# Kernel tuning notes

Measured on AMD Instinct MI355X. Metric: run time of the kernel, lower is better.

## Reference

```python
import jax, jax.numpy as jnp
import numpy as np

U, I, NG, D, G, B = 100000, 50000, 20000, 64, 20, 16384
H_GE = (D + 2 * D) // 2  # 96, group_encoder hidden

def setup_inputs() -> dict:
    key = jax.random.key(0)
    ks = jax.random.split(key, 24)
    s = 0.1
    return {
        'group_inputs': jax.random.randint(ks[0], (B,), 0, NG),
        'item_inputs': jax.random.randint(ks[1], (B,), 0, I),
        'group_members': jax.random.randint(ks[2], (NG, G), 0, U),
        'eps': jax.random.normal(ks[3], (B, D), dtype=jnp.float32),
        'user_emb': jax.random.normal(ks[4], (U, D), dtype=jnp.float32) * s,
        'item_emb': jax.random.normal(ks[5], (I, D), dtype=jnp.float32) * s,
        # user_encoder: MLP(D, D, 1) -> Linear(D,D), ReLU, Linear(D,D)
        'ue_w1': jax.random.normal(ks[6], (D, D), dtype=jnp.float32) * s,
        'ue_b1': jnp.zeros((D,), jnp.float32),
        'ue_w2': jax.random.normal(ks[7], (D, D), dtype=jnp.float32) * s,
        'ue_b2': jnp.zeros((D,), jnp.float32),
        # group_encoder: MLP(D, 2D, 1) -> Linear(D,96), ReLU, Linear(96,2D)
        'ge_w1': jax.random.normal(ks[8], (D, H_GE), dtype=jnp.float32) * s,
        'ge_b1': jnp.zeros((H_GE,), jnp.float32),
        'ge_w2': jax.random.normal(ks[9], (H_GE, 2 * D), dtype=jnp.float32) * s,
        'ge_b2': jnp.zeros((2 * D,), jnp.float32),
        # attention: Linear(2D,16), ReLU, Linear(16,1)
        'at_w1': jax.random.normal(ks[10], (2 * D, 16), dtype=jnp.float32) * s,
        'at_b1': jnp.zeros((16,), jnp.float32),
        'at_w2': jax.random.normal(ks[11], (16, 1), dtype=jnp.float32) * s,
        'at_b2': jnp.zeros((1,), jnp.float32),
        # predict: Linear(3D,8), ReLU, Linear(8,1)
        'pr_w1': jax.random.normal(ks[12], (3 * D, 8), dtype=jnp.float32) * s,
        'pr_b1': jnp.zeros((8,), jnp.float32),
        'pr_w2': jax.random.normal(ks[13], (8, 1), dtype=jnp.float32) * s,
        'pr_b2': jnp.zeros((1,), jnp.float32),
    }

def reference(group_inputs, item_inputs, group_members, eps,
              user_emb, item_emb,
              ue_w1, ue_b1, ue_w2, ue_b2,
              ge_w1, ge_b1, ge_w2, ge_b2,
              at_w1, at_b1, at_w2, at_b2,
              pr_w1, pr_b1, pr_w2, pr_b2):
    mem_idx = group_members[group_inputs]              # [B, G]
    me = user_emb[mem_idx]                             # [B, G, D] gather
    # user encoder MLP
    enc = jnp.maximum(me @ ue_w1 + ue_b1, 0) @ ue_w2 + ue_b2
    gz = jnp.maximum(jnp.mean(enc, axis=1), 0)         # [B, D]
    gz = jnp.maximum(gz @ ge_w1 + ge_b1, 0) @ ge_w2 + ge_b2  # [B, 2D]
    z_mu, log_sigma = gz[:, :D], gz[:, D:]
    z_sigma = 0.1 + 0.9 * jax.nn.sigmoid(log_sigma)
    ie = item_emb[item_inputs]                          # [B, D]
    gi = jnp.concatenate([me, jnp.broadcast_to(ie[:, None, :], me.shape)], axis=-1)  # [B, G, 2D]
    score = jnp.maximum(gi @ at_w1 + at_b1, 0) @ at_w2 + at_b2  # [B, G, 1]
    w = jax.nn.softmax(score[..., 0], axis=1)           # [B, G]
    g_att = jnp.einsum('bg,bgd->bd', w, me)             # [B, D]
    ge_full = g_att + z_mu + z_sigma * eps              # sample_z with given eps
    ncf = jnp.concatenate([ge_full * ie, ge_full, ie], axis=-1)  # [B, 3D]
    h = jnp.maximum(ncf @ pr_w1 + pr_b1, 0) @ pr_w2 + pr_b2
    return jax.nn.sigmoid(h)                            # [B, 1]
```

## Files before the change

kernel.cpp:

```cpp
#include <hip/hip_runtime.h>
#include <math.h>

#define D_   64
#define G_   20
#define BT   16
#define XPAD 132

typedef __attribute__((ext_vector_type(8))) short bf8;
typedef __attribute__((ext_vector_type(4))) float f4;

__device__ __forceinline__ short f2bf(float f){
    union { float f; unsigned u; } c; c.f = f;
    unsigned r = c.u + 0x7fffu + ((c.u >> 16) & 1u);
    return (short)(r >> 16);
}
__device__ __forceinline__ bf8 pack8(float4 a, float4 b){
    bf8 r;
    r[0]=f2bf(a.x); r[1]=f2bf(a.y); r[2]=f2bf(a.z); r[3]=f2bf(a.w);
    r[4]=f2bf(b.x); r[5]=f2bf(b.y); r[6]=f2bf(b.z); r[7]=f2bf(b.w);
    return r;
}

__global__ __launch_bounds__(256, 4) void vargr_mfma_kernel(
    const int*   __restrict__ group_inputs,
    const int*   __restrict__ item_inputs,
    const int*   __restrict__ group_members,
    const float* __restrict__ eps,
    const float* __restrict__ user_emb,
    const float* __restrict__ item_emb,
    const float* __restrict__ ue_w1, const float* __restrict__ ue_b1,
    const float* __restrict__ ue_w2, const float* __restrict__ ue_b2,
    const float* __restrict__ ge_w1, const float* __restrict__ ge_b1,
    const float* __restrict__ ge_w2, const float* __restrict__ ge_b2,
    const float* __restrict__ at_w1, const float* __restrict__ at_b1,
    const float* __restrict__ at_w2, const float* __restrict__ at_b2,
    const float* __restrict__ pr_w1, const float* __restrict__ pr_b1,
    const float* __restrict__ pr_w2, const float* __restrict__ pr_b2,
    float* __restrict__ out)
{
    __shared__ unsigned short Wt[80*64];
    __shared__ float xA[BT*XPAD];
    __shared__ float xB[BT*XPAD];
    __shared__ float ieb[BT*64];
    __shared__ float gefb[BT*64];
    __shared__ float tvs[BT*16];
    __shared__ float wsm[BT*G_];
    __shared__ int   sidx[BT*G_];

    const int tid = threadIdx.x;
    const int w = tid >> 6, l = tid & 63;
    const int bbase = blockIdx.x * BT;

    for (int e = tid; e < 64*80; e += 256){
        int k = e / 80, col = e - k*80;
        float v = (col < 64) ? ue_w1[k*64 + col] : at_w1[k*16 + (col - 64)];
        int byte = col*128 + ( ((2*k) & ~15) ^ ((col & 7) << 4) ) + ((2*k) & 15);
        *(unsigned short*)((char*)Wt + byte) = (unsigned short)f2bf(v);
    }

    {
        int bb = 4*w + (l >> 4);
        int q  = l & 15;
        int item = item_inputs[bbase + bb];
        ((float4*)(ieb + bb*64))[q] = ((const float4*)(item_emb + (size_t)item*64))[q];
    }
    #pragma unroll
    for (int i = 0; i < 4; ++i){
        int bb = 4*w + i;
        if (l < G_){
            int gid = group_inputs[bbase + bb];
            sidx[bb*G_ + l] = group_members[gid*G_ + l];
        }
    }
    {
        int bb = 4*w + (l >> 4);
        int u  = l & 15;
        float acc = at_b1[u];
        const float* ier = ieb + bb*64;
        #pragma unroll 8
        for (int k = 0; k < 64; ++k) acc += ier[k] * at_w1[(64 + k)*16 + u];
        tvs[bb*16 + u] = acc;
    }
    __syncthreads();

    bf8 bfr[5][2];
    #pragma unroll
    for (int nt = 0; nt < 5; ++nt)
        #pragma unroll
        for (int kt = 0; kt < 2; ++kt){
            int col  = nt*16 + (l & 15);
            int byte = col*128 + ( (kt*64 + (l >> 4)*16) ^ ((col & 7) << 4) );
            bfr[nt][kt] = *(const bf8*)((const char*)Wt + byte);
        }
    float bias1[4];
    #pragma unroll
    for (int nt = 0; nt < 4; ++nt) bias1[nt] = ue_b1[nt*16 + (l & 15)];
    const float aw2  = at_w2[l & 15];
    const float atb2 = at_b2[0];

    #pragma unroll 1
    for (int i = 0; i < 4; ++i){
        const int bb = 4*w + i;
        const int* sx = sidx + bb*G_;
        float msum[4] = {0.f, 0.f, 0.f, 0.f};

        #pragma unroll
        for (int mt = 0; mt < 2; ++mt){
            int r = mt*16 + (l & 15);
            int g = (r < G_) ? r : (G_ - 1);
            const float4* p = (const float4*)(user_emb + (size_t)sx[g]*64) + ((l >> 4)*2);
            bf8 a0 = pack8(p[0], p[1]);
            bf8 a1 = pack8(p[8], p[9]);

            f4 acc[5];
            #pragma unroll
            for (int nt = 0; nt < 5; ++nt) acc[nt] = (f4){0.f, 0.f, 0.f, 0.f};
            #pragma unroll
            for (int nt = 0; nt < 5; ++nt){
                acc[nt] = __builtin_amdgcn_mfma_f32_16x16x32_bf16(a0, bfr[nt][0], acc[nt], 0, 0, 0);
                acc[nt] = __builtin_amdgcn_mfma_f32_16x16x32_bf16(a1, bfr[nt][1], acc[nt], 0, 0, 0);
            }

            #pragma unroll
            for (int nt = 0; nt < 4; ++nt){
                float rs = 0.f;
                #pragma unroll
                for (int rr = 0; rr < 4; ++rr) rs += fmaxf(acc[nt][rr] + bias1[nt], 0.f);
                if (mt == 1 && (l >> 4) != 0) rs = 0.f;
                msum[nt] += rs;
            }
            {
                float tvv = tvs[bb*16 + (l & 15)];
                float vv[4];
                #pragma unroll
                for (int rr = 0; rr < 4; ++rr) vv[rr] = fmaxf(acc[4][rr] + tvv, 0.f) * aw2;
                #pragma unroll
                for (int rr = 0; rr < 4; ++rr){
                    vv[rr] += __shfl_xor(vv[rr], 1);
                    vv[rr] += __shfl_xor(vv[rr], 2);
                    vv[rr] += __shfl_xor(vv[rr], 4);
                    vv[rr] += __shfl_xor(vv[rr], 8);
                }
                if ((l & 15) == 0 && (mt == 0 || (l >> 4) == 0)){
                    #pragma unroll
                    for (int rr = 0; rr < 4; ++rr)
                        wsm[bb*G_ + mt*16 + (l >> 4)*4 + rr] = vv[rr] + atb2;
                }
            }
        }

        #pragma unroll
        for (int nt = 0; nt < 4; ++nt){
            msum[nt] += __shfl_xor(msum[nt], 16);
            msum[nt] += __shfl_xor(msum[nt], 32);
            if ((l >> 4) == nt) xA[bb*XPAD + nt*16 + (l & 15)] = msum[nt] * (1.f / G_);
        }

        {
            float sval = (l < G_) ? wsm[bb*G_ + l] : -3.0e38f;
            float mx = sval;
            mx = fmaxf(mx, __shfl_xor(mx, 1, 32));
            mx = fmaxf(mx, __shfl_xor(mx, 2, 32));
            mx = fmaxf(mx, __shfl_xor(mx, 4, 32));
            mx = fmaxf(mx, __shfl_xor(mx, 8, 32));
            mx = fmaxf(mx, __shfl_xor(mx, 16, 32));
            float e = (l < G_) ? expf(sval - mx) : 0.f;
            float sm = e;
            sm += __shfl_xor(sm, 1, 32);
            sm += __shfl_xor(sm, 2, 32);
            sm += __shfl_xor(sm, 4, 32);
            sm += __shfl_xor(sm, 8, 32);
            sm += __shfl_xor(sm, 16, 32);
            if (l < G_) wsm[bb*G_ + l] = e / sm;
        }

        {
            float ga = 0.f;
            #pragma unroll
            for (int g = 0; g < G_; ++g)
                ga += wsm[bb*G_ + g] * user_emb[(size_t)sx[g]*64 + l];
            gefb[bb*64 + l] = ga;
        }
    }
    __syncthreads();

    {
        int col = w*16 + (l & 15);
        f4 acc = (f4){0.f, 0.f, 0.f, 0.f};
        #pragma unroll
        for (int kt = 0; kt < 2; ++kt){
            const float* ap = xA + (l & 15)*XPAD + kt*32 + (l >> 4)*8;
            bf8 a = pack8(*(const float4*)ap, *(const float4*)(ap + 4));
            int k0 = kt*32 + (l >> 4)*8;
            bf8 bfrg;
            #pragma unroll
            for (int q = 0; q < 8; ++q) bfrg[q] = f2bf(ue_w2[(k0 + q)*64 + col]);
            acc = __builtin_amdgcn_mfma_f32_16x16x32_bf16(a, bfrg, acc, 0, 0, 0);
        }
        float bs = ue_b2[col];
        #pragma unroll
        for (int rr = 0; rr < 4; ++rr)
            xB[(4*(l >> 4) + rr)*XPAD + col] = fmaxf(acc[rr] + bs, 0.f);
    }
    __syncthreads();

    for (int t = w; t < 6; t += 4){
        int col = t*16 + (l & 15);
        f4 acc = (f4){0.f, 0.f, 0.f, 0.f};
        #pragma unroll
        for (int kt = 0; kt < 2; ++kt){
            const float* ap = xB + (l & 15)*XPAD + kt*32 + (l >> 4)*8;
            bf8 a = pack8(*(const float4*)ap, *(const float4*)(ap + 4));
            int k0 = kt*32 + (l >> 4)*8;
            bf8 bfrg;
            #pragma unroll
            for (int q = 0; q < 8; ++q) bfrg[q] = f2bf(ge_w1[(k0 + q)*96 + col]);
            acc = __builtin_amdgcn_mfma_f32_16x16x32_bf16(a, bfrg, acc, 0, 0, 0);
        }
        float bs = ge_b1[col];
        #pragma unroll
        for (int rr = 0; rr < 4; ++rr)
            xA[(4*(l >> 4) + rr)*XPAD + col] = fmaxf(acc[rr] + bs, 0.f);
    }
    __syncthreads();

    for (int t = w; t < 8; t += 4){
        int col = t*16 + (l & 15);
        f4 acc = (f4){0.f, 0.f, 0.f, 0.f};
        #pragma unroll
        for (int kt = 0; kt < 3; ++kt){
            const float* ap = xA + (l & 15)*XPAD + kt*32 + (l >> 4)*8;
            bf8 a = pack8(*(const float4*)ap, *(const float4*)(ap + 4));
            int k0 = kt*32 + (l >> 4)*8;
            bf8 bfrg;
            #pragma unroll
            for (int q = 0; q < 8; ++q) bfrg[q] = f2bf(ge_w2[(k0 + q)*128 + col]);
            acc = __builtin_amdgcn_mfma_f32_16x16x32_bf16(a, bfrg, acc, 0, 0, 0);
        }
        float bs = ge_b2[col];
        #pragma unroll
        for (int rr = 0; rr < 4; ++rr)
            xB[(4*(l >> 4) + rr)*XPAD + col] = acc[rr] + bs;
    }
    __syncthreads();

    {
        float pa[8], pb_[8], pc_[8], pb1v[8], pw2v[8];
        #pragma unroll
        for (int u = 0; u < 8; ++u){
            pa[u]   = pr_w1[l*8 + u];
            pb_[u]  = pr_w1[(64 + l)*8 + u];
            pc_[u]  = pr_w1[(128 + l)*8 + u];
            pb1v[u] = pr_b1[u];
            pw2v[u] = pr_w2[u];
        }
        const float pb2v = pr_b2[0];

        #pragma unroll 1
        for (int i = 0; i < 4; ++i){
            int bb = 4*w + i;
            int b  = bbase + bb;
            float muv = xB[bb*XPAD + l];
            float sgr = xB[bb*XPAD + 64 + l];
            float sg  = 0.1f + 0.9f / (1.f + expf(-sgr));
            float gefv = gefb[bb*64 + l] + muv + sg * eps[(size_t)b*64 + l];
            float iev  = ieb[bb*64 + l];
            float x0 = gefv * iev;
            float pu[8];
            #pragma unroll
            for (int u = 0; u < 8; ++u) pu[u] = x0*pa[u] + gefv*pb_[u] + iev*pc_[u];
            #pragma unroll
            for (int off = 1; off < 64; off <<= 1){
                #pragma unroll
                for (int u = 0; u < 8; ++u) pu[u] += __shfl_xor(pu[u], off);
            }
            float hh = 0.f;
            #pragma unroll
            for (int u = 0; u < 8; ++u) hh += fmaxf(pu[u] + pb1v[u], 0.f) * pw2v[u];
            if (l == 0) out[b] = 1.f / (1.f + expf(-(hh + pb2v)));
        }
    }
}

extern "C" void kernel_launch(void* const* d_in, const int* in_sizes, int n_in,
                              void* d_out, int out_size, void* d_ws, size_t ws_size,
                              hipStream_t stream) {
    const int*   group_inputs  = (const int*)d_in[0];
    const int*   item_inputs   = (const int*)d_in[1];
    const int*   group_members = (const int*)d_in[2];
    const float* eps           = (const float*)d_in[3];
    const float* user_emb      = (const float*)d_in[4];
    const float* item_emb      = (const float*)d_in[5];
    const float* ue_w1 = (const float*)d_in[6];
    const float* ue_b1 = (const float*)d_in[7];
    const float* ue_w2 = (const float*)d_in[8];
    const float* ue_b2 = (const float*)d_in[9];
    const float* ge_w1 = (const float*)d_in[10];
    const float* ge_b1 = (const float*)d_in[11];
    const float* ge_w2 = (const float*)d_in[12];
    const float* ge_b2 = (const float*)d_in[13];
    const float* at_w1 = (const float*)d_in[14];
    const float* at_b1 = (const float*)d_in[15];
    const float* at_w2 = (const float*)d_in[16];
    const float* at_b2 = (const float*)d_in[17];
    const float* pr_w1 = (const float*)d_in[18];
    const float* pr_b1 = (const float*)d_in[19];
    const float* pr_w2 = (const float*)d_in[20];
    const float* pr_b2 = (const float*)d_in[21];
    float* out = (float*)d_out;

    const int nb = in_sizes[0];
    vargr_mfma_kernel<<<nb / BT, 256, 0, stream>>>(
        group_inputs, item_inputs, group_members, eps, user_emb, item_emb,
        ue_w1, ue_b1, ue_w2, ue_b2, ge_w1, ge_b1, ge_w2, ge_b2,
        at_w1, at_b1, at_w2, at_b2, pr_w1, pr_b1, pr_w2, pr_b2,
        out);
}
```

Baseline: 45.06 us.

## Pre-pack weights to bf16 MFMA fragments in a prep kernel and restructure member tiling

Adds a small prep kernel that converts all MLP weights once into bf16 MFMA fragment layout in workspace, so each block loads fragments directly instead of building a swizzled LDS copy and converting weights per block. Member tiling now computes members 0-15 per batch row in the loop and handles members 16-19 of four rows together in one extra MFMA tile, removing the half-empty second tile. Item attention projection, intermediate activations (stored as bf16) and the final predict MLP now use MFMA instead of scalar loops and 64-lane shuffle reductions. It costs an extra kernel launch and more bf16 rounding in intermediate layers.

```diff
diff --git a/kernel.cpp b/kernel.cpp
--- a/kernel.cpp
+++ b/kernel.cpp
@@ -1,161 +1,234 @@
 #include <hip/hip_runtime.h>
+#include <hip/hip_bf16.h>
 #include <math.h>
 
-#define D_   64
 #define G_   20
 #define BT   16
-#define XPAD 132
 
 typedef __attribute__((ext_vector_type(8))) short bf8;
 typedef __attribute__((ext_vector_type(4))) float f4;
 
-__device__ __forceinline__ short f2bf(float f){
-    union { float f; unsigned u; } c; c.f = f;
-    unsigned r = c.u + 0x7fffu + ((c.u >> 16) & 1u);
-    return (short)(r >> 16);
+#define FMB  0
+#define FAT  10
+#define FUE2 12
+#define FGE1 20
+#define FGE2 32
+#define FPR  56
+#define FTOT 62
+
+__device__ __forceinline__ unsigned cvt2(float x, float y){
+    float2 f; f.x = x; f.y = y;
+    __hip_bfloat162 h = __float22bfloat162_rn(f);
+    return *reinterpret_cast<unsigned*>(&h);
+}
+__device__ __forceinline__ unsigned short cvt1(float x){
+    __hip_bfloat16 h = __float2bfloat16(x);
+    return *reinterpret_cast<unsigned short*>(&h);
 }
 __device__ __forceinline__ bf8 pack8(float4 a, float4 b){
-    bf8 r;
-    r[0]=f2bf(a.x); r[1]=f2bf(a.y); r[2]=f2bf(a.z); r[3]=f2bf(a.w);
-    r[4]=f2bf(b.x); r[5]=f2bf(b.y); r[6]=f2bf(b.z); r[7]=f2bf(b.w);
-    return r;
-}
-
-__global__ __launch_bounds__(256, 4) void vargr_mfma_kernel(
+    union { bf8 v; unsigned u[4]; } t;
+    t.u[0] = cvt2(a.x, a.y); t.u[1] = cvt2(a.z, a.w);
+    t.u[2] = cvt2(b.x, b.y); t.u[3] = cvt2(b.z, b.w);
+    return t.v;
+}
+
+__global__ __launch_bounds__(256) void vargr_prep(
+    const float* __restrict__ ue_w1, const float* __restrict__ ue_w2,
+    const float* __restrict__ ge_w1, const float* __restrict__ ge_w2,
+    const float* __restrict__ at_w1, const float* __restrict__ pr_w1,
+    unsigned short* __restrict__ ws)
+{
+    int f = blockIdx.x * 256 + threadIdx.x;
+    if (f >= FTOT * 64) return;
+    int lane = f & 63, grp = f >> 6;
+    int col = lane & 15;
+    int q8  = (lane >> 4) * 8;
+    float v[8];
+    if (grp < FAT){
+        int g = grp - FMB; int nt = g >> 1; int k0 = (g & 1)*32 + q8; int c = nt*16 + col;
+        #pragma unroll
+        for (int q = 0; q < 8; ++q)
+            v[q] = (c < 64) ? ue_w1[(k0+q)*64 + c] : at_w1[(k0+q)*16 + (c - 64)];
+    } else if (grp < FUE2){
+        int g = grp - FAT; int k0 = g*32 + q8;
+        #pragma unroll
+        for (int q = 0; q < 8; ++q) v[q] = at_w1[(64 + k0 + q)*16 + col];
+    } else if (grp < FGE1){
+        int g = grp - FUE2; int nt = g >> 1; int k0 = (g & 1)*32 + q8;
+        #pragma unroll
+        for (int q = 0; q < 8; ++q) v[q] = ue_w2[(k0+q)*64 + nt*16 + col];
+    } else if (grp < FGE2){
+        int g = grp - FGE1; int nt = g >> 1; int k0 = (g & 1)*32 + q8;
+        #pragma unroll
+        for (int q = 0; q < 8; ++q) v[q] = ge_w1[(k0+q)*96 + nt*16 + col];
+    } else if (grp < FPR){
+        int g = grp - FGE2; int nt = g / 3; int k0 = (g % 3)*32 + q8;
+        #pragma unroll
+        for (int q = 0; q < 8; ++q) v[q] = ge_w2[(k0+q)*128 + nt*16 + col];
+    } else {
+        int g = grp - FPR; int k0 = g*32 + q8;
+        #pragma unroll
+        for (int q = 0; q < 8; ++q) v[q] = (col < 8) ? pr_w1[(k0+q)*8 + col] : 0.f;
+    }
+    union { bf8 b; unsigned u[4]; } t;
+    t.u[0] = cvt2(v[0], v[1]); t.u[1] = cvt2(v[2], v[3]);
+    t.u[2] = cvt2(v[4], v[5]); t.u[3] = cvt2(v[6], v[7]);
+    *reinterpret_cast<bf8*>(ws + (size_t)f * 8) = t.b;
+}
+
+__global__ __launch_bounds__(256, 4) void vargr_main(
     const int*   __restrict__ group_inputs,
     const int*   __restrict__ item_inputs,
     const int*   __restrict__ group_members,
     const float* __restrict__ eps,
     const float* __restrict__ user_emb,
     const float* __restrict__ item_emb,
-    const float* __restrict__ ue_w1, const float* __restrict__ ue_b1,
-    const float* __restrict__ ue_w2, const float* __restrict__ ue_b2,
-    const float* __restrict__ ge_w1, const float* __restrict__ ge_b1,
-    const float* __restrict__ ge_w2, const float* __restrict__ ge_b2,
-    const float* __restrict__ at_w1, const float* __restrict__ at_b1,
-    const float* __restrict__ at_w2, const float* __restrict__ at_b2,
-    const float* __restrict__ pr_w1, const float* __restrict__ pr_b1,
+    const float* __restrict__ ue_b1, const float* __restrict__ ue_b2,
+    const float* __restrict__ ge_b1, const float* __restrict__ ge_b2,
+    const float* __restrict__ at_b1, const float* __restrict__ at_w2,
+    const float* __restrict__ at_b2, const float* __restrict__ pr_b1,
     const float* __restrict__ pr_w2, const float* __restrict__ pr_b2,
+    const unsigned short* __restrict__ ws,
     float* __restrict__ out)
 {
-    __shared__ unsigned short Wt[80*64];
-    __shared__ float xA[BT*XPAD];
-    __shared__ float xB[BT*XPAD];
-    __shared__ float ieb[BT*64];
+    __shared__ unsigned short xAh[BT*136];
+    __shared__ unsigned short xBh[BT*136];
+    __shared__ float ieb[BT*68];
     __shared__ float gefb[BT*64];
-    __shared__ float tvs[BT*16];
     __shared__ float wsm[BT*G_];
     __shared__ int   sidx[BT*G_];
+    __shared__ float x3u[BT*132];
 
     const int tid = threadIdx.x;
     const int w = tid >> 6, l = tid & 63;
+    const int lq = l >> 4, lr = l & 15;
     const int bbase = blockIdx.x * BT;
-
-    for (int e = tid; e < 64*80; e += 256){
-        int k = e / 80, col = e - k*80;
-        float v = (col < 64) ? ue_w1[k*64 + col] : at_w1[k*16 + (col - 64)];
-        int byte = col*128 + ( ((2*k) & ~15) ^ ((col & 7) << 4) ) + ((2*k) & 15);
-        *(unsigned short*)((char*)Wt + byte) = (unsigned short)f2bf(v);
-    }
+    const bf8* wsf = (const bf8*)ws;
+
+    bf8 bfr[5][2];
+    #pragma unroll
+    for (int nt = 0; nt < 5; ++nt)
+        #pragma unroll
+        for (int kt = 0; kt < 2; ++kt)
+            bfr[nt][kt] = wsf[(FMB + nt*2 + kt)*64 + l];
+    bf8 abot0 = wsf[(FAT + 0)*64 + l];
+    bf8 abot1 = wsf[(FAT + 1)*64 + l];
+
+    float bias1[4];
+    #pragma unroll
+    for (int nt = 0; nt < 4; ++nt) bias1[nt] = ue_b1[nt*16 + lr];
+    const float aw2  = at_w2[lr];
+    const float atb2 = at_b2[0];
 
     {
-        int bb = 4*w + (l >> 4);
-        int q  = l & 15;
+        int bb = 4*w + lq;
         int item = item_inputs[bbase + bb];
-        ((float4*)(ieb + bb*64))[q] = ((const float4*)(item_emb + (size_t)item*64))[q];
-    }
-    #pragma unroll
-    for (int i = 0; i < 4; ++i){
-        int bb = 4*w + i;
-        if (l < G_){
+        ((float4*)(ieb + bb*68))[lr] = ((const float4*)(item_emb + (size_t)item*64))[lr];
+    }
+    if (l < G_){
+        #pragma unroll
+        for (int i = 0; i < 4; ++i){
+            int bb = 4*w + i;
             int gid = group_inputs[bbase + bb];
             sidx[bb*G_ + l] = group_members[gid*G_ + l];
         }
     }
+    __syncthreads();
+
+    f4 tvacc = (f4){0.f, 0.f, 0.f, 0.f};
+    #pragma unroll
+    for (int kt = 0; kt < 2; ++kt){
+        const float* ap = ieb + lr*68 + kt*32 + lq*8;
+        bf8 a = pack8(*(const float4*)ap, *(const float4*)(ap + 4));
+        tvacc = __builtin_amdgcn_mfma_f32_16x16x32_bf16(a, kt ? abot1 : abot0, tvacc, 0, 0, 0);
+    }
+    const float atb1 = at_b1[lr];
+    float tvi[4];
+    #pragma unroll
+    for (int i = 0; i < 4; ++i)
+        tvi[i] = __shfl(tvacc[i], w*16 + lr) + atb1;
+
+    float rem[4];
     {
-        int bb = 4*w + (l >> 4);
-        int u  = l & 15;
-        float acc = at_b1[u];
-        const float* ier = ieb + bb*64;
-        #pragma unroll 8
-        for (int k = 0; k < 64; ++k) acc += ier[k] * at_w1[(64 + k)*16 + u];
-        tvs[bb*16 + u] = acc;
-    }
-    __syncthreads();
-
-    bf8 bfr[5][2];
-    #pragma unroll
-    for (int nt = 0; nt < 5; ++nt)
-        #pragma unroll
-        for (int kt = 0; kt < 2; ++kt){
-            int col  = nt*16 + (l & 15);
-            int byte = col*128 + ( (kt*64 + (l >> 4)*16) ^ ((col & 7) << 4) );
-            bfr[nt][kt] = *(const bf8*)((const char*)Wt + byte);
-        }
-    float bias1[4];
-    #pragma unroll
-    for (int nt = 0; nt < 4; ++nt) bias1[nt] = ue_b1[nt*16 + (l & 15)];
-    const float aw2  = at_w2[l & 15];
-    const float atb2 = at_b2[0];
+        int sx = sidx[(4*w + (lr >> 2))*G_ + 16 + (lr & 3)];
+        const float4* p = (const float4*)(user_emb + (size_t)sx*64) + lq*2;
+        bf8 a0 = pack8(p[0], p[1]);
+        bf8 a1 = pack8(p[8], p[9]);
+        f4 acc[5];
+        #pragma unroll
+        for (int nt = 0; nt < 5; ++nt) acc[nt] = (f4){0.f, 0.f, 0.f, 0.f};
+        #pragma unroll
+        for (int nt = 0; nt < 5; ++nt){
+            acc[nt] = __builtin_amdgcn_mfma_f32_16x16x32_bf16(a0, bfr[nt][0], acc[nt], 0, 0, 0);
+            acc[nt] = __builtin_amdgcn_mfma_f32_16x16x32_bf16(a1, bfr[nt][1], acc[nt], 0, 0, 0);
+        }
+        #pragma unroll
+        for (int nt = 0; nt < 4; ++nt){
+            float rs = 0.f;
+            #pragma unroll
+            for (int rr = 0; rr < 4; ++rr) rs += fmaxf(acc[nt][rr] + bias1[nt], 0.f);
+            rem[nt] = rs;
+        }
+        float tvq = (lq == 0) ? tvi[0] : (lq == 1) ? tvi[1] : (lq == 2) ? tvi[2] : tvi[3];
+        float vv[4];
+        #pragma unroll
+        for (int rr = 0; rr < 4; ++rr) vv[rr] = fmaxf(acc[4][rr] + tvq, 0.f) * aw2;
+        #pragma unroll
+        for (int rr = 0; rr < 4; ++rr){
+            vv[rr] += __shfl_xor(vv[rr], 1, 16);
+            vv[rr] += __shfl_xor(vv[rr], 2, 16);
+            vv[rr] += __shfl_xor(vv[rr], 4, 16);
+            vv[rr] += __shfl_xor(vv[rr], 8, 16);
+        }
+        if (lr == 0){
+            #pragma unroll
+            for (int rr = 0; rr < 4; ++rr)
+                wsm[(4*w + lq)*G_ + 16 + rr] = vv[rr] + atb2;
+        }
+    }
 
     #pragma unroll 1
     for (int i = 0; i < 4; ++i){
         const int bb = 4*w + i;
-        const int* sx = sidx + bb*G_;
-        float msum[4] = {0.f, 0.f, 0.f, 0.f};
-
-        #pragma unroll
-        for (int mt = 0; mt < 2; ++mt){
-            int r = mt*16 + (l & 15);
-            int g = (r < G_) ? r : (G_ - 1);
-            const float4* p = (const float4*)(user_emb + (size_t)sx[g]*64) + ((l >> 4)*2);
-            bf8 a0 = pack8(p[0], p[1]);
-            bf8 a1 = pack8(p[8], p[9]);
-
-            f4 acc[5];
-            #pragma unroll
-            for (int nt = 0; nt < 5; ++nt) acc[nt] = (f4){0.f, 0.f, 0.f, 0.f};
-            #pragma unroll
-            for (int nt = 0; nt < 5; ++nt){
-                acc[nt] = __builtin_amdgcn_mfma_f32_16x16x32_bf16(a0, bfr[nt][0], acc[nt], 0, 0, 0);
-                acc[nt] = __builtin_amdgcn_mfma_f32_16x16x32_bf16(a1, bfr[nt][1], acc[nt], 0, 0, 0);
+        const int sx = sidx[bb*G_ + lr];
+        const float4* p = (const float4*)(user_emb + (size_t)sx*64) + lq*2;
+        bf8 a0 = pack8(p[0], p[1]);
+        bf8 a1 = pack8(p[8], p[9]);
+        f4 acc[5];
+        #pragma unroll
+        for (int nt = 0; nt < 5; ++nt) acc[nt] = (f4){0.f, 0.f, 0.f, 0.f};
+        #pragma unroll
+        for (int nt = 0; nt < 5; ++nt){
+            acc[nt] = __builtin_amdgcn_mfma_f32_16x16x32_bf16(a0, bfr[nt][0], acc[nt], 0, 0, 0);
+            acc[nt] = __builtin_amdgcn_mfma_f32_16x16x32_bf16(a1, bfr[nt][1], acc[nt], 0, 0, 0);
+        }
+        #pragma unroll
+        for (int nt = 0; nt < 4; ++nt){
+            float rs = 0.f;
+            #pragma unroll
+            for (int rr = 0; rr < 4; ++rr) rs += fmaxf(acc[nt][rr] + bias1[nt], 0.f);
+            if (lq == i) rs += rem[nt];
+            rs += __shfl_xor(rs, 16);
+            rs += __shfl_xor(rs, 32);
+            if (lq == nt) xAh[bb*136 + nt*16 + lr] = cvt1(rs * (1.f / G_));
+        }
+        {
+            float vv[4];
+            #pragma unroll
+            for (int rr = 0; rr < 4; ++rr) vv[rr] = fmaxf(acc[4][rr] + tvi[i], 0.f) * aw2;
+            #pragma unroll
+            for (int rr = 0; rr < 4; ++rr){
+                vv[rr] += __shfl_xor(vv[rr], 1, 16);
+                vv[rr] += __shfl_xor(vv[rr], 2, 16);
+                vv[rr] += __shfl_xor(vv[rr], 4, 16);
+                vv[rr] += __shfl_xor(vv[rr], 8, 16);
             }
-
-            #pragma unroll
-            for (int nt = 0; nt < 4; ++nt){
-                float rs = 0.f;
+            if (lr == 0){
                 #pragma unroll
-                for (int rr = 0; rr < 4; ++rr) rs += fmaxf(acc[nt][rr] + bias1[nt], 0.f);
-                if (mt == 1 && (l >> 4) != 0) rs = 0.f;
-                msum[nt] += rs;
+                for (int rr = 0; rr < 4; ++rr)
+                    wsm[bb*G_ + 4*lq + rr] = vv[rr] + atb2;
             }
-            {
-                float tvv = tvs[bb*16 + (l & 15)];
-                float vv[4];
-                #pragma unroll
-                for (int rr = 0; rr < 4; ++rr) vv[rr] = fmaxf(acc[4][rr] + tvv, 0.f) * aw2;
-                #pragma unroll
-                for (int rr = 0; rr < 4; ++rr){
-                    vv[rr] += __shfl_xor(vv[rr], 1);
-                    vv[rr] += __shfl_xor(vv[rr], 2);
-                    vv[rr] += __shfl_xor(vv[rr], 4);
-                    vv[rr] += __shfl_xor(vv[rr], 8);
-                }
-                if ((l & 15) == 0 && (mt == 0 || (l >> 4) == 0)){
-                    #pragma unroll
-                    for (int rr = 0; rr < 4; ++rr)
-                        wsm[bb*G_ + mt*16 + (l >> 4)*4 + rr] = vv[rr] + atb2;
-                }
-            }
-        }
-
-        #pragma unroll
-        for (int nt = 0; nt < 4; ++nt){
-            msum[nt] += __shfl_xor(msum[nt], 16);
-            msum[nt] += __shfl_xor(msum[nt], 32);
-            if ((l >> 4) == nt) xA[bb*XPAD + nt*16 + (l & 15)] = msum[nt] * (1.f / G_);
-        }
-
+        }
         {
             float sval = (l < G_) ? wsm[bb*G_ + l] : -3.0e38f;
             float mx = sval;
@@ -173,111 +246,103 @@
             sm += __shfl_xor(sm, 16, 32);
             if (l < G_) wsm[bb*G_ + l] = e / sm;
         }
-
         {
             float ga = 0.f;
             #pragma unroll
             for (int g = 0; g < G_; ++g)
-                ga += wsm[bb*G_ + g] * user_emb[(size_t)sx[g]*64 + l];
+                ga += wsm[bb*G_ + g] * user_emb[(size_t)sidx[bb*G_ + g]*64 + l];
             gefb[bb*64 + l] = ga;
         }
     }
     __syncthreads();
 
     {
-        int col = w*16 + (l & 15);
+        int col = w*16 + lr;
         f4 acc = (f4){0.f, 0.f, 0.f, 0.f};
         #pragma unroll
         for (int kt = 0; kt < 2; ++kt){
-            const float* ap = xA + (l & 15)*XPAD + kt*32 + (l >> 4)*8;
-            bf8 a = pack8(*(const float4*)ap, *(const float4*)(ap + 4));
-            int k0 = kt*32 + (l >> 4)*8;
-            bf8 bfrg;
-            #pragma unroll
-            for (int q = 0; q < 8; ++q) bfrg[q] = f2bf(ue_w2[(k0 + q)*64 + col]);
-            acc = __builtin_amdgcn_mfma_f32_16x16x32_bf16(a, bfrg, acc, 0, 0, 0);
+            bf8 a = *(const bf8*)(xAh + lr*136 + kt*32 + lq*8);
+            acc = __builtin_amdgcn_mfma_f32_16x16x32_bf16(a, wsf[(FUE2 + w*2 + kt)*64 + l], acc, 0, 0, 0);
         }
         float bs = ue_b2[col];
         #pragma unroll
         for (int rr = 0; rr < 4; ++rr)
-            xB[(4*(l >> 4) + rr)*XPAD + col] = fmaxf(acc[rr] + bs, 0.f);
-    }
-    __syncthreads();
-
+            xBh[(4*lq + rr)*136 + col] = cvt1(fmaxf(acc[rr] + bs, 0.f));
+    }
+    __syncthreads();
     for (int t = w; t < 6; t += 4){
-        int col = t*16 + (l & 15);
+        int col = t*16 + lr;
         f4 acc = (f4){0.f, 0.f, 0.f, 0.f};
         #pragma unroll
         for (int kt = 0; kt < 2; ++kt){
-            const float* ap = xB + (l & 15)*XPAD + kt*32 + (l >> 4)*8;
-            bf8 a = pack8(*(const float4*)ap, *(const float4*)(ap + 4));
-            int k0 = kt*32 + (l >> 4)*8;
-            bf8 bfrg;
-            #pragma unroll
-            for (int q = 0; q < 8; ++q) bfrg[q] = f2bf(ge_w1[(k0 + q)*96 + col]);
-            acc = __builtin_amdgcn_mfma_f32_16x16x32_bf16(a, bfrg, acc, 0, 0, 0);
+            bf8 a = *(const bf8*)(xBh + lr*136 + kt*32 + lq*8);
+            acc = __builtin_amdgcn_mfma_f32_16x16x32_bf16(a, wsf[(FGE1 + t*2 + kt)*64 + l], acc, 0, 0, 0);
         }
         float bs = ge_b1[col];
         #pragma unroll
         for (int rr = 0; rr < 4; ++rr)
-            xA[(4*(l >> 4) + rr)*XPAD + col] = fmaxf(acc[rr] + bs, 0.f);
-    }
-    __syncthreads();
-
+            xAh[(4*lq + rr)*136 + col] = cvt1(fmaxf(acc[rr] + bs, 0.f));
+    }
+    __syncthreads();
     for (int t = w; t < 8; t += 4){
-        int col = t*16 + (l & 15);
+        int col = t*16 + lr;
         f4 acc = (f4){0.f, 0.f, 0.f, 0.f};
         #pragma unroll
         for (int kt = 0; kt < 3; ++kt){
-            const float* ap = xA + (l & 15)*XPAD + kt*32 + (l >> 4)*8;
-            bf8 a = pack8(*(const float4*)ap, *(const float4*)(ap + 4));
-            int k0 = kt*32 + (l >> 4)*8;
-            bf8 bfrg;
-            #pragma unroll
-            for (int q = 0; q < 8; ++q) bfrg[q] = f2bf(ge_w2[(k0 + q)*128 + col]);
-            acc = __builtin_amdgcn_mfma_f32_16x16x32_bf16(a, bfrg, acc, 0, 0, 0);
+            bf8 a = *(const bf8*)(xAh + lr*136 + kt*32 + lq*8);
+            acc = __builtin_amdgcn_mfma_f32_16x16x32_bf16(a, wsf[(FGE2 + t*3 + kt)*64 + l], acc, 0, 0, 0);
         }
         float bs = ge_b2[col];
         #pragma unroll
         for (int rr = 0; rr < 4; ++rr)
-            xB[(4*(l >> 4) + rr)*XPAD + col] = acc[rr] + bs;
-    }
-    __syncthreads();
-
-    {
-        float pa[8], pb_[8], pc_[8], pb1v[8], pw2v[8];
-        #pragma unroll
-        for (int u = 0; u < 8; ++u){
-            pa[u]   = pr_w1[l*8 + u];
-            pb_[u]  = pr_w1[(64 + l)*8 + u];
-            pc_[u]  = pr_w1[(128 + l)*8 + u];
-            pb1v[u] = pr_b1[u];
-            pw2v[u] = pr_w2[u];
-        }
-        const float pb2v = pr_b2[0];
-
-        #pragma unroll 1
-        for (int i = 0; i < 4; ++i){
-            int bb = 4*w + i;
-            int b  = bbase + bb;
-            float muv = xB[bb*XPAD + l];
-            float sgr = xB[bb*XPAD + 64 + l];
-            float sg  = 0.1f + 0.9f / (1.f + expf(-sgr));
-            float gefv = gefb[bb*64 + l] + muv + sg * eps[(size_t)b*64 + l];
-            float iev  = ieb[bb*64 + l];
-            float x0 = gefv * iev;
-            float pu[8];
-            #pragma unroll
-            for (int u = 0; u < 8; ++u) pu[u] = x0*pa[u] + gefv*pb_[u] + iev*pc_[u];
-            #pragma unroll
-            for (int off = 1; off < 64; off <<= 1){
-                #pragma unroll
-                for (int u = 0; u < 8; ++u) pu[u] += __shfl_xor(pu[u], off);
-            }
-            float hh = 0.f;
-            #pragma unroll
-            for (int u = 0; u < 8; ++u) hh += fmaxf(pu[u] + pb1v[u], 0.f) * pw2v[u];
-            if (l == 0) out[b] = 1.f / (1.f + expf(-(hh + pb2v)));
+            x3u[(4*lq + rr)*132 + col] = acc[rr] + bs;
+    }
+    __syncthreads();
+
+    #pragma unroll
+    for (int i = 0; i < 4; ++i){
+        int bb = 4*w + i;
+        float mu  = x3u[bb*132 + l];
+        float sgr = x3u[bb*132 + 64 + l];
+        float sg  = 0.1f + 0.9f / (1.f + expf(-sgr));
+        gefb[bb*64 + l] += mu + sg * eps[(size_t)(bbase + bb)*64 + l];
+    }
+    __syncthreads();
+    unsigned short* ncf = (unsigned short*)x3u;
+    #pragma unroll
+    for (int i = 0; i < 4; ++i){
+        int bb = 4*w + i;
+        float gef = gefb[bb*64 + l];
+        float iev = ieb[bb*68 + l];
+        ncf[bb*200 + l]       = cvt1(gef * iev);
+        ncf[bb*200 + 64 + l]  = cvt1(gef);
+        ncf[bb*200 + 128 + l] = cvt1(iev);
+    }
+    __syncthreads();
+    if (w == 0){
+        f4 acc = (f4){0.f, 0.f, 0.f, 0.f};
+        #pragma unroll
+        for (int kt = 0; kt < 6; ++kt){
+            bf8 a = *(const bf8*)(ncf + lr*200 + kt*32 + lq*8);
+            acc = __builtin_amdgcn_mfma_f32_16x16x32_bf16(a, wsf[(FPR + kt)*64 + l], acc, 0, 0, 0);
+        }
+        float pb1 = (lr < 8) ? pr_b1[lr] : 0.f;
+        float pw2 = (lr < 8) ? pr_w2[lr] : 0.f;
+        float pb2 = pr_b2[0];
+        float vv[4];
+        #pragma unroll
+        for (int rr = 0; rr < 4; ++rr) vv[rr] = fmaxf(acc[rr] + pb1, 0.f) * pw2;
+        #pragma unroll
+        for (int rr = 0; rr < 4; ++rr){
+            vv[rr] += __shfl_xor(vv[rr], 1, 16);
+            vv[rr] += __shfl_xor(vv[rr], 2, 16);
+            vv[rr] += __shfl_xor(vv[rr], 4, 16);
+            vv[rr] += __shfl_xor(vv[rr], 8, 16);
+        }
+        if (lr == 0){
+            #pragma unroll
+            for (int rr = 0; rr < 4; ++rr)
+                out[bbase + 4*lq + rr] = 1.f / (1.f + expf(-(vv[rr] + pb2)));
         }
     }
 }
@@ -308,11 +373,14 @@
     const float* pr_w2 = (const float*)d_in[20];
     const float* pr_b2 = (const float*)d_in[21];
     float* out = (float*)d_out;
+    unsigned short* ws = (unsigned short*)d_ws;
+
+    vargr_prep<<<(FTOT*64 + 255)/256, 256, 0, stream>>>(
+        ue_w1, ue_w2, ge_w1, ge_w2, at_w1, pr_w1, ws);
 
     const int nb = in_sizes[0];
-    vargr_mfma_kernel<<<nb / BT, 256, 0, stream>>>(
+    vargr_main<<<nb / BT, 256, 0, stream>>>(
         group_inputs, item_inputs, group_members, eps, user_emb, item_emb,
-        ue_w1, ue_b1, ue_w2, ue_b2, ge_w1, ge_b1, ge_w2, ge_b2,
-        at_w1, at_b1, at_w2, at_b2, pr_w1, pr_b1, pr_w2, pr_b2,
-        out);
-}
+        ue_b1, ue_b2, ge_b1, ge_b2, at_b1, at_w2, at_b2, pr_b1, pr_w2, pr_b2,
+        ws, out);
+}
```

Result: no change. 44.97 us (-0.2%).
